# Kernel tuning notes

Measured on AMD Instinct MI355X. Metric: run time of the kernel, lower is better.

The kernel has to match this reference:

```python
import jax, jax.numpy as jnp
import numpy as np

B, N_ATOMS = 64, 127            # graphs, atoms per graph (uniform)
L = N_ATOMS + 1                 # +1 cls token
D_MODEL, NHEAD, NUM_LAYERS, D_FF = 1024, 16, 8, 3072
HEAD_DIM = D_MODEL // NHEAD
MAX_TOKENS = 131                # 121 + 10
NEIGH_VOCAB = 14 + 3            # max_neighbors + 3
DIST_VOCAB = 83 + 3             # max_distance + 3
EPS = 1e-5


def _dist_bins():
    # short_cutoff=0.9, long_cutoff=5.0, precision=0.05; first 3 edges overridden
    b = np.arange(0.9 - 3 * 0.05, 5.0, 0.05)
    b[:3] = [-1.0, 0.0, 0.01]
    return jnp.asarray(b, jnp.float32)  # len 85 -> digitize indices in [0, 85]


def _layer_norm(x, g, b):
    m = jnp.mean(x, -1, keepdims=True)
    v = jnp.var(x, -1, keepdims=True)
    return (x - m) * jax.lax.rsqrt(v + EPS) * g + b


def setup_inputs() -> dict:
    key = jax.random.key(0)
    ks = jax.random.split(key, 16)
    s = 0.02
    z = jax.random.randint(ks[0], (B * N_ATOMS,), 0, 119)
    hgs = jax.random.randint(ks[1], (B * N_ATOMS,), 0, 15)
    pos = jax.random.normal(ks[2], (B * N_ATOMS, 3), jnp.float32) * 3.0
    batch = jnp.repeat(jnp.arange(B, dtype=jnp.int64), N_ATOMS)
    atoms_emb = (jax.random.normal(ks[3], (MAX_TOKENS, D_MODEL), jnp.float32) * s).at[0].set(0.0)  # padding_idx=0
    neigh_emb = (jax.random.normal(ks[4], (NEIGH_VOCAB, D_MODEL), jnp.float32) * s).at[0].set(0.0)
    dist_emb = jax.random.normal(ks[5], (DIST_VOCAB, NHEAD), jnp.float32) * s  # row 0 forced to -inf in reference
    Wqkv = jax.random.normal(ks[6], (D_MODEL, 3 * D_MODEL), jnp.float32) * s
    bqkv = jnp.zeros((3 * D_MODEL,), jnp.float32)
    Wo = jax.random.normal(ks[7], (D_MODEL, D_MODEL), jnp.float32) * s
    bo = jnp.zeros((D_MODEL,), jnp.float32)
    W1 = jax.random.normal(ks[8], (D_MODEL, D_FF), jnp.float32) * s
    b1f = jnp.zeros((D_FF,), jnp.float32)
    W2 = jax.random.normal(ks[9], (D_FF, D_MODEL), jnp.float32) * s
    b2f = jnp.zeros((D_MODEL,), jnp.float32)
    ln1_g = jnp.ones((D_MODEL,), jnp.float32); ln1_b = jnp.zeros((D_MODEL,), jnp.float32)
    ln2_g = jnp.ones((D_MODEL,), jnp.float32); ln2_b = jnp.zeros((D_MODEL,), jnp.float32)
    return dict(z=z, hgs=hgs, pos=pos, batch=batch, atoms_emb=atoms_emb, neigh_emb=neigh_emb,
                dist_emb=dist_emb, Wqkv=Wqkv, bqkv=bqkv, Wo=Wo, bo=bo,
                W1=W1, b1f=b1f, W2=W2, b2f=b2f,
                ln1_g=ln1_g, ln1_b=ln1_b, ln2_g=ln2_g, ln2_b=ln2_b)


def reference(z, hgs, pos, batch, atoms_emb, neigh_emb, dist_emb,
              Wqkv, bqkv, Wo, bo, W1, b1f, W2, b2f, ln1_g, ln1_b, ln2_g, ln2_b):
    # batch is uniform (N_ATOMS per graph, sorted), so per-graph batching == reshape
    zb = z.reshape(B, N_ATOMS).astype(jnp.int32) + 2
    hb = hgs.reshape(B, N_ATOMS).astype(jnp.int32) + 2
    atoms = jnp.concatenate([jnp.ones((B, 1), jnp.int32), zb], axis=1)        # cls token = 1
    neighbors = jnp.concatenate([jnp.zeros((B, 1), jnp.int32), hb], axis=1)   # cls neighbors = 0

    p = pos.reshape(B, N_ATOMS, 3)
    dist = jnp.sqrt(jnp.sum((p[:, None, :, :] - p[:, :, None, :]) ** 2, axis=-1))  # (B,n,n)
    didx = jnp.digitize(dist, _dist_bins()).astype(jnp.int32)                      # self-loop -> 2
    distances = jnp.ones((B, L, L), jnp.int32).at[:, 1:, 1:].set(didx)             # cls row/col = 1

    # neg_inf_idx=0 padding mask row (unused here since no padding -> indices >= 1)
    w_d = dist_emb.at[0].set(-jnp.inf)
    d_mask = w_d[distances].transpose(0, 3, 1, 2)  # (B, H, L, L)

    x = atoms_emb[atoms] + neigh_emb[neighbors]    # (B, L, D)
    scale = 1.0 / jnp.sqrt(jnp.float32(HEAD_DIM))
    for _ in range(NUM_LAYERS):  # shared weights + shared attention bias
        qkv = x @ Wqkv + bqkv
        q, k, v = jnp.split(qkv, 3, axis=-1)
        q = q.reshape(B, L, NHEAD, HEAD_DIM)
        k = k.reshape(B, L, NHEAD, HEAD_DIM)
        v = v.reshape(B, L, NHEAD, HEAD_DIM)
        scores = jnp.einsum('blhd,bmhd->bhlm', q, k) * scale + d_mask
        a = jax.nn.softmax(scores, axis=-1)
        o = jnp.einsum('bhlm,bmhd->blhd', a, v).reshape(B, L, D_MODEL) @ Wo + bo
        x = _layer_norm(x + o, ln1_g, ln1_b)                      # post-norm (norm_first=False)
        h = jax.nn.gelu(x @ W1 + b1f, approximate=False) @ W2 + b2f
        x = _layer_norm(x + h, ln2_g, ln2_b)
    return x[:, 0]  # cls embedding, (B, D_MODEL)
```

## Files before the change

kernel.cpp:

```cpp
#include <hip/hip_runtime.h>
#include <cstdint>
#include <math.h>

typedef unsigned short u16;
typedef __attribute__((ext_vector_type(4))) float f32x4;
typedef __attribute__((ext_vector_type(8))) __bf16 bf16x8;
typedef __attribute__((ext_vector_type(8))) short short8;

typedef __attribute__((address_space(1))) void g_void;
typedef __attribute__((address_space(3))) void l_void;

__device__ __forceinline__ u16 f2bf(float f) {
  uint32_t u = __builtin_bit_cast(uint32_t, f);
  u += 0x7FFFu + ((u >> 16) & 1u);
  return (u16)(u >> 16);
}
__device__ __forceinline__ float bf2f(u16 h) {
  uint32_t u = ((uint32_t)h) << 16;
  return __builtin_bit_cast(float, u);
}

__device__ __forceinline__ void gload16(const void* g, void* l) {
  __builtin_amdgcn_global_load_lds((g_void*)g, (l_void*)l, 16, 0, 0);
}

__device__ __forceinline__ float gelu_exact(float x) {
  float a = x * 0.70710678118654752f;
  float s = fabsf(a);
  float t = __builtin_amdgcn_rcpf(fmaf(0.3275911f, s, 1.0f));
  float p = fmaf(fmaf(fmaf(fmaf(1.061405429f, t, -1.453152027f), t, 1.421413741f), t,
                      -0.284496736f), t, 0.254829592f);
  p *= t;
  float e = __expf(-s * s);
  float er = fmaf(-p, e, 1.0f);
  er = copysignf(er, a);
  return 0.5f * x * (1.0f + er);
}

__global__ void transpose_w(const float* __restrict__ W, u16* __restrict__ Wt, int K, int N) {
  __shared__ float t[32][33];
  const int nb = blockIdx.x * 32, kb = blockIdx.y * 32;
  const int tx = threadIdx.x, ty = threadIdx.y;
#pragma unroll
  for (int i = 0; i < 32; i += 8)
    t[ty + i][tx] = W[(size_t)(kb + ty + i) * N + nb + tx];
  __syncthreads();
#pragma unroll
  for (int i = 0; i < 32; i += 8)
    Wt[(size_t)(nb + ty + i) * K + kb + tx] = f2bf(t[tx][ty + i]);
}

__global__ void embed_k(const int* __restrict__ z, const int* __restrict__ hgs,
                        const float* __restrict__ ae, const float* __restrict__ ne,
                        u16* __restrict__ xb) {
  const int row = blockIdx.x;
  const int b = row >> 7, tl = row & 127;
  int ia = 1, in_ = 0;
  if (tl > 0) { ia = z[b * 127 + tl - 1] + 2; in_ = hgs[b * 127 + tl - 1] + 2; }
  const float* ar = ae + (size_t)ia * 1024;
  const float* nr = ne + (size_t)in_ * 1024;
  for (int c = threadIdx.x; c < 1024; c += 256)
    xb[(size_t)row * 1024 + c] = f2bf(ar[c] + nr[c]);
}

__global__ void mask_k(const float* __restrict__ pos, const float* __restrict__ demb,
                       u16* __restrict__ mask) {
  __shared__ float edges[85];
  __shared__ float dh[86 * 16];
  const int bq = blockIdx.x;
  const int b = bq >> 7, lq = bq & 127;
  const int lk = threadIdx.x;
  if (lk < 85) {
    double e = 0.75 + 0.05 * (double)lk;
    float ef = (float)e;
    if (lk == 0) ef = -1.0f; else if (lk == 1) ef = 0.0f; else if (lk == 2) ef = 0.01f;
    edges[lk] = ef;
  }
  for (int i = lk; i < 86 * 16; i += 128) {
    float v = demb[i];
    if (i < 16) v = -INFINITY;
    dh[i] = v;
  }
  __syncthreads();
  int c;
  if (lq == 0 || lk == 0) {
    c = 1;
  } else {
    const float* pi = pos + ((size_t)b * 127 + lq - 1) * 3;
    const float* pj = pos + ((size_t)b * 127 + lk - 1) * 3;
    const float dx = pi[0] - pj[0], dy = pi[1] - pj[1], dz = pi[2] - pj[2];
    const float d = sqrtf(dx * dx + dy * dy + dz * dz);
    int cnt = 0;
#pragma unroll
    for (int k2 = 0; k2 < 85; ++k2) cnt += (edges[k2] <= d) ? 1 : 0;
    c = cnt;
  }
  const int fr = lk & 15, nn = lk >> 4;
#pragma unroll
  for (int h = 0; h < 16; ++h)
    mask[((((size_t)(b * 16 + h) * 16 + fr) * 128 + lq) << 3) + nn] = f2bf(dh[c * 16 + h]);
}

template <int MODE>
__launch_bounds__(512, 4)
__global__ void gemmS(const u16* __restrict__ A, const u16* __restrict__ Bt,
                      const float* __restrict__ bias,
                      u16* __restrict__ O0, u16* __restrict__ O1, u16* __restrict__ O2,
                      int N, int K) {
  extern __shared__ char lds[];
  constexpr int SLAB = 24576;
  const int tid = threadIdx.x;
  const int w = tid >> 6, l = tid & 63;
  const int wr = w >> 1, wc = w & 1;
  const int nwg = gridDim.x;
  const int wg = (blockIdx.x & 7) * (nwg >> 3) + (blockIdx.x >> 3);
  const int ntn = N >> 7;
  const int bm = wg / ntn, bn = wg - (wg / ntn) * ntn;
  const int NT = K >> 5;

  const int colc = ((((l & 3) << 4) ^ (((l >> 2) & 8) << 2)) >> 1);
  const u16* Ag = A + (size_t)(bm * 256 + w * 16 + (l >> 2)) * K + colc;
  const u16* Bg = Bt + (size_t)(bn * 128 + w * 16 + (l >> 2)) * K + colc;
  const int ldst = w << 10;

  auto stage = [&](int t, char* buf) {
    const int kb = t << 5;
    gload16(Ag + kb, buf + ldst);
    gload16(Ag + (size_t)128 * K + kb, buf + 8192 + ldst);
    gload16(Bg + kb, buf + 16384 + ldst);
  };

  const int lo = ((l & 15) << 6) + (((l >> 4) << 4) ^ ((l & 8) << 2));

  f32x4 acc[4][4];
#pragma unroll
  for (int m = 0; m < 4; ++m)
#pragma unroll
    for (int n = 0; n < 4; ++n) acc[m][n] = f32x4{0.f, 0.f, 0.f, 0.f};

  char* p0 = lds;
  char* p1 = lds + SLAB;
  char* p2 = lds + 2 * SLAB;

  stage(0, p0);
  stage(1, p1);
  asm volatile("s_waitcnt vmcnt(3)" ::: "memory");
  __builtin_amdgcn_s_barrier();

  for (int t = 0; t < NT; ++t) {
    if (t + 2 < NT) stage(t + 2, p2);
    const char* ab = p0 + (wr << 12);
    const char* bb = p0 + 16384 + (wc << 12);
    bf16x8 af[4], bf[4];
#pragma unroll
    for (int m = 0; m < 4; ++m) af[m] = *(const bf16x8*)(ab + (m << 10) + lo);
#pragma unroll
    for (int n = 0; n < 4; ++n) bf[n] = *(const bf16x8*)(bb + (n << 10) + lo);
    __builtin_amdgcn_s_setprio(1);
#pragma unroll
    for (int m = 0; m < 4; ++m)
#pragma unroll
      for (int n = 0; n < 4; ++n)
        acc[m][n] = __builtin_amdgcn_mfma_f32_16x16x32_bf16(af[m], bf[n], acc[m][n], 0, 0, 0);
    __builtin_amdgcn_s_setprio(0);
    if (t + 2 < NT) asm volatile("s_waitcnt vmcnt(3)" ::: "memory");
    else            asm volatile("s_waitcnt vmcnt(0)" ::: "memory");
    __builtin_amdgcn_s_barrier();
    char* tmp = p0; p0 = p1; p1 = p2; p2 = tmp;
  }

  const int fr = l & 15, fq = l >> 4;
  const int colb = bn * 128 + wc * 64;
  const int rowb = bm * 256 + wr * 64;
  float bv[4];
#pragma unroll
  for (int n = 0; n < 4; ++n) bv[n] = bias[colb + n * 16 + fr];
  const int region = colb >> 10;

#pragma unroll
  for (int m = 0; m < 4; ++m) {
#pragma unroll
    for (int n = 0; n < 4; ++n) {
      const int col = colb + n * 16 + fr;
      if (MODE == 0 && region == 2) {
        const int row0_ = rowb + m * 16 + fq * 4;
        const int bI = row0_ >> 7, tl0 = row0_ & 127;
        const int c = col & 1023, h = c >> 6, d = c & 63;
        ushort4 pk;
        pk.x = f2bf(acc[m][n][0] + bv[n]);
        pk.y = f2bf(acc[m][n][1] + bv[n]);
        pk.z = f2bf(acc[m][n][2] + bv[n]);
        pk.w = f2bf(acc[m][n][3] + bv[n]);
        *(ushort4*)&O2[(((size_t)bI * 16 + h) * 64 + d) * 128 + tl0] = pk;
      } else {
#pragma unroll
        for (int j = 0; j < 4; ++j) {
          const int row = rowb + m * 16 + fq * 4 + j;
          float v = acc[m][n][j] + bv[n];
          if (MODE == 2) v = gelu_exact(v);
          if (MODE == 0) {
            const int bI = row >> 7, tl = row & 127;
            const int c = col & 1023, h = c >> 6, d = c & 63;
            if (region == 0) O0[(((size_t)bI * 16 + h) * 128 + tl) * 64 + d] = f2bf(v);
            else             O1[(((size_t)bI * 16 + h) * 128 + tl) * 64 + d] = f2bf(v);
          } else {
            O0[(size_t)row * N + col] = f2bf(v);
          }
        }
      }
    }
  }
}

__launch_bounds__(256, 3)
__global__ void gemm4(const u16* __restrict__ A, const u16* __restrict__ Bt,
                      const float* __restrict__ bias, u16* __restrict__ O,
                      int N, int K) {
  extern __shared__ char lds[];
  constexpr int SLAB = 16384;
  const int tid = threadIdx.x;
  const int w = tid >> 6, l = tid & 63;
  const int wr = w >> 1, wc = w & 1;
  const int nwg = gridDim.x;
  const int wg = (blockIdx.x & 7) * (nwg >> 3) + (blockIdx.x >> 3);
  const int ntn = N >> 7;
  const int bm = wg / ntn, bn = wg - (wg / ntn) * ntn;
  const int NT = K >> 5;

  const int colc = ((((l & 3) << 4) ^ (((l >> 2) & 8) << 2)) >> 1);
  const u16* Ag = A + (size_t)(bm * 128 + w * 16 + (l >> 2)) * K + colc;
  const u16* Bg = Bt + (size_t)(bn * 128 + w * 16 + (l >> 2)) * K + colc;
  const int ldst = w << 10;

  auto stage = [&](int t, char* buf) {
    const int kb = t << 5;
    gload16(Ag + kb, buf + ldst);
    gload16(Ag + (size_t)64 * K + kb, buf + 4096 + ldst);
    gload16(Bg + kb, buf + 8192 + ldst);
    gload16(Bg + (size_t)64 * K + kb, buf + 12288 + ldst);
  };

  const int lo = ((l & 15) << 6) + (((l >> 4) << 4) ^ ((l & 8) << 2));

  f32x4 acc[4][4];
#pragma unroll
  for (int m = 0; m < 4; ++m)
#pragma unroll
    for (int n = 0; n < 4; ++n) acc[m][n] = f32x4{0.f, 0.f, 0.f, 0.f};

  char* p0 = lds;
  char* p1 = lds + SLAB;
  char* p2 = lds + 2 * SLAB;

  stage(0, p0);
  stage(1, p1);
  asm volatile("s_waitcnt vmcnt(4)" ::: "memory");
  __builtin_amdgcn_s_barrier();

  for (int t = 0; t < NT; ++t) {
    if (t + 2 < NT) stage(t + 2, p2);
    const char* ab = p0 + (wr << 12);
    const char* bb = p0 + 8192 + (wc << 12);
    bf16x8 af[4], bf[4];
#pragma unroll
    for (int m = 0; m < 4; ++m) af[m] = *(const bf16x8*)(ab + (m << 10) + lo);
#pragma unroll
    for (int n = 0; n < 4; ++n) bf[n] = *(const bf16x8*)(bb + (n << 10) + lo);
    __builtin_amdgcn_s_setprio(1);
#pragma unroll
    for (int m = 0; m < 4; ++m)
#pragma unroll
      for (int n = 0; n < 4; ++n)
        acc[m][n] = __builtin_amdgcn_mfma_f32_16x16x32_bf16(af[m], bf[n], acc[m][n], 0, 0, 0);
    __builtin_amdgcn_s_setprio(0);
    if (t + 2 < NT) asm volatile("s_waitcnt vmcnt(4)" ::: "memory");
    else            asm volatile("s_waitcnt vmcnt(0)" ::: "memory");
    __builtin_amdgcn_s_barrier();
    char* tmp = p0; p0 = p1; p1 = p2; p2 = tmp;
  }

  const int fr = l & 15, fq = l >> 4;
  const int colb = bn * 128 + wc * 64;
  const int rowb = bm * 128 + wr * 64;
  float bv[4];
#pragma unroll
  for (int n = 0; n < 4; ++n) bv[n] = bias[colb + n * 16 + fr];
#pragma unroll
  for (int m = 0; m < 4; ++m)
#pragma unroll
    for (int n = 0; n < 4; ++n) {
      const int col = colb + n * 16 + fr;
#pragma unroll
      for (int j = 0; j < 4; ++j) {
        const int row = rowb + m * 16 + fq * 4 + j;
        O[(size_t)row * N + col] = f2bf(acc[m][n][j] + bv[n]);
      }
    }
}

__launch_bounds__(256)
__global__ void attn_kernel(const u16* __restrict__ Qg, const u16* __restrict__ Kg,
                            const u16* __restrict__ Vg,
                            const u16* __restrict__ mask,
                            u16* __restrict__ Og) {
  __shared__ u16 QK[2 * 128 * 64];
  __shared__ u16 Vt[64 * 128];
  const int tid = threadIdx.x;
  const int wv = tid >> 6;
  const int l = tid & 63;
  const int bh = blockIdx.x;
  const int b = bh >> 4;

  const char* Qs = (const char*)(Qg + (size_t)bh * 8192);
  const char* Ks = (const char*)(Kg + (size_t)bh * 8192);
  const char* Vs = (const char*)(Vg + (size_t)bh * 8192);
  char* QKb = (char*)QK;
  char* Vtb = (char*)Vt;
#pragma unroll
  for (int it = 0; it < 4; ++it) {
    const int r = it * 32 + (tid >> 3);
    const int cb = (tid & 7) * 16;
    const int sw = cb ^ ((r & 7) << 4);
    *(uint4*)(QKb + r * 128 + sw) = *(const uint4*)(Qs + r * 128 + cb);
    *(uint4*)(QKb + 16384 + r * 128 + sw) = *(const uint4*)(Ks + r * 128 + cb);
  }
#pragma unroll
  for (int it = 0; it < 4; ++it) {
    const int r = it * 16 + (tid >> 4);
    const int cb = (tid & 15) * 16;
    const int sw = cb ^ ((r & 7) << 4);
    *(uint4*)(Vtb + r * 256 + sw) = *(const uint4*)(Vs + r * 256 + cb);
  }
  __syncthreads();

  f32x4 s[2][8];
#pragma unroll
  for (int m = 0; m < 2; ++m)
#pragma unroll
    for (int n = 0; n < 8; ++n) s[m][n] = f32x4{0.f, 0.f, 0.f, 0.f};
#pragma unroll
  for (int kk = 0; kk < 2; ++kk) {
    bf16x8 qa[2], kb[8];
#pragma unroll
    for (int m = 0; m < 2; ++m) {
      const int qr = wv * 32 + m * 16 + (l & 15);
      qa[m] = *(const bf16x8*)(QKb + qr * 128 + ((kk * 64 + (l >> 4) * 16) ^ ((qr & 7) << 4)));
    }
#pragma unroll
    for (int n = 0; n < 8; ++n) {
      const int kr = n * 16 + (l & 15);
      kb[n] = *(const bf16x8*)(QKb + 16384 + kr * 128 + ((kk * 64 + (l >> 4) * 16) ^ ((kr & 7) << 4)));
    }
#pragma unroll
    for (int m = 0; m < 2; ++m)
#pragma unroll
      for (int n = 0; n < 8; ++n)
        s[m][n] = __builtin_amdgcn_mfma_f32_16x16x32_bf16(qa[m], kb[n], s[m][n], 0, 0, 0);
  }

  const u16* mb2 = mask + (((size_t)bh * 16 + (l & 15)) << 10);
  float rinv[2][4];
#pragma unroll
  for (int m = 0; m < 2; ++m) {
#pragma unroll
    for (int j = 0; j < 4; ++j) {
      const int lq = wv * 32 + m * 16 + (l >> 4) * 4 + j;
      const short8 mv = *(const short8*)(mb2 + lq * 8);
      float vals[8];
#pragma unroll
      for (int n = 0; n < 8; ++n)
        vals[n] = fmaf(s[m][n][j], 0.125f, bf2f((u16)mv[n]));
      float mx = vals[0];
#pragma unroll
      for (int n = 1; n < 8; ++n) mx = fmaxf(mx, vals[n]);
#pragma unroll
      for (int o = 1; o < 16; o <<= 1) mx = fmaxf(mx, __shfl_xor(mx, o, 64));
      float sum = 0.f;
#pragma unroll
      for (int n = 0; n < 8; ++n) { vals[n] = expf(vals[n] - mx); sum += vals[n]; }
#pragma unroll
      for (int o = 1; o < 16; o <<= 1) sum += __shfl_xor(sum, o, 64);
      rinv[m][j] = 1.f / sum;
#pragma unroll
      for (int n = 0; n < 8; ++n) s[m][n][j] = vals[n];
    }
  }
  __syncthreads();
  char* Pb = QKb + wv * 8192;
#pragma unroll
  for (int m = 0; m < 2; ++m)
#pragma unroll
    for (int n = 0; n < 8; ++n)
#pragma unroll
      for (int j = 0; j < 4; ++j) {
        const int pr = m * 16 + (l >> 4) * 4 + j;
        const int pc = (n * 16 + (l & 15)) * 2;
        *(u16*)(Pb + pr * 256 + (pc ^ ((pr & 7) << 4))) = f2bf(s[m][n][j]);
      }
  __syncthreads();

  f32x4 o_[2][4];
#pragma unroll
  for (int m = 0; m < 2; ++m)
#pragma unroll
    for (int n = 0; n < 4; ++n) o_[m][n] = f32x4{0.f, 0.f, 0.f, 0.f};
#pragma unroll
  for (int ks = 0; ks < 4; ++ks) {
    bf16x8 pa[2], vb[4];
#pragma unroll
    for (int m = 0; m < 2; ++m) {
      const int pr = m * 16 + (l & 15);
      pa[m] = *(const bf16x8*)(Pb + pr * 256 + ((ks * 64 + (l >> 4) * 16) ^ ((pr & 7) << 4)));
    }
#pragma unroll
    for (int n = 0; n < 4; ++n) {
      const int vr = n * 16 + (l & 15);
      vb[n] = *(const bf16x8*)(Vtb + vr * 256 + ((ks * 64 + (l >> 4) * 16) ^ ((vr & 7) << 4)));
    }
#pragma unroll
    for (int m = 0; m < 2; ++m)
#pragma unroll
      for (int n = 0; n < 4; ++n)
        o_[m][n] = __builtin_amdgcn_mfma_f32_16x16x32_bf16(pa[m], vb[n], o_[m][n], 0, 0, 0);
  }
  const int h = bh & 15;
#pragma unroll
  for (int m = 0; m < 2; ++m)
#pragma unroll
    for (int n = 0; n < 4; ++n)
#pragma unroll
      for (int j = 0; j < 4; ++j) {
        const int lo2 = wv * 32 + m * 16 + (l >> 4) * 4 + j;
        const int d = n * 16 + (l & 15);
        Og[((size_t)b * 128 + lo2) * 1024 + h * 64 + d] = f2bf(o_[m][n][j] * rinv[m][j]);
      }
}

__launch_bounds__(256)
__global__ void ln_res(u16* __restrict__ xb, const u16* __restrict__ o,
                       const float* __restrict__ gam, const float* __restrict__ bet,
                       float* __restrict__ cls_out) {
  const int row = blockIdx.x * 4 + (threadIdx.x >> 6);
  const int l = threadIdx.x & 63;
  const size_t base = (size_t)row * 1024 + l * 16;
  const int c0 = l * 16;
  float v[16], gv[16], bb[16];
  const short8 xa = *(const short8*)(xb + base);
  const short8 xc = *(const short8*)(xb + base + 8);
  const short8 oa = *(const short8*)(o + base);
  const short8 oc = *(const short8*)(o + base + 8);
#pragma unroll
  for (int i = 0; i < 4; ++i) {
    *(float4*)&gv[i * 4] = *(const float4*)(gam + c0 + i * 4);
    *(float4*)&bb[i * 4] = *(const float4*)(bet + c0 + i * 4);
  }
  float s = 0.f, sq = 0.f;
#pragma unroll
  for (int i = 0; i < 8; ++i) {
    v[i] = bf2f((u16)xa[i]) + bf2f((u16)oa[i]);
    v[i + 8] = bf2f((u16)xc[i]) + bf2f((u16)oc[i]);
  }
#pragma unroll
  for (int i = 0; i < 16; ++i) { s += v[i]; sq += v[i] * v[i]; }
#pragma unroll
  for (int off = 1; off < 64; off <<= 1) {
    s += __shfl_xor(s, off, 64);
    sq += __shfl_xor(sq, off, 64);
  }
  const float mean = s * (1.f / 1024.f);
  const float var = sq * (1.f / 1024.f) - mean * mean;
  const float rstd = rsqrtf(var + 1e-5f);
  short8 ra, rc;
#pragma unroll
  for (int i = 0; i < 8; ++i) {
    const float ya = (v[i] - mean) * rstd * gv[i] + bb[i];
    const float yc = (v[i + 8] - mean) * rstd * gv[i + 8] + bb[i + 8];
    ra[i] = (short)f2bf(ya);
    rc[i] = (short)f2bf(yc);
    if ((row & 127) == 0) {
      cls_out[(size_t)(row >> 7) * 1024 + c0 + i] = ya;
      cls_out[(size_t)(row >> 7) * 1024 + c0 + 8 + i] = yc;
    }
  }
  *(short8*)(xb + base) = ra;
  *(short8*)(xb + base + 8) = rc;
}

extern "C" void kernel_launch(void* const* d_in, const int* in_sizes, int n_in,
                              void* d_out, int out_size, void* d_ws, size_t ws_size,
                              hipStream_t stream) {
  const int* z = (const int*)d_in[0];
  const int* hgs = (const int*)d_in[1];
  const float* pos = (const float*)d_in[2];
  const float* atoms_emb = (const float*)d_in[4];
  const float* neigh_emb = (const float*)d_in[5];
  const float* dist_emb = (const float*)d_in[6];
  const float* Wqkv = (const float*)d_in[7];
  const float* bqkv = (const float*)d_in[8];
  const float* Wo = (const float*)d_in[9];
  const float* bo = (const float*)d_in[10];
  const float* W1 = (const float*)d_in[11];
  const float* b1f = (const float*)d_in[12];
  const float* W2 = (const float*)d_in[13];
  const float* b2f = (const float*)d_in[14];
  const float* ln1g = (const float*)d_in[15];
  const float* ln1b = (const float*)d_in[16];
  const float* ln2g = (const float*)d_in[17];
  const float* ln2b = (const float*)d_in[18];

  size_t off = 0;
  char* wsb = (char*)d_ws;
  auto alc = [&](size_t bytes) { void* p = wsb + off; off += (bytes + 255) & ~(size_t)255; return p; };
  u16* xb = (u16*)alc(8192ull * 1024 * 2);
  u16* q = (u16*)alc(8192ull * 1024 * 2);
  u16* k = (u16*)alc(8192ull * 1024 * 2);
  u16* v = (u16*)alc(8192ull * 1024 * 2);
  u16* proj = (u16*)alc(8192ull * 1024 * 2);
  u16* big = (u16*)alc(8192ull * 3072 * 2);
  u16* wqkvt = (u16*)alc(3072ull * 1024 * 2);
  u16* wot = (u16*)alc(1024ull * 1024 * 2);
  u16* w1t = (u16*)alc(3072ull * 1024 * 2);
  u16* w2t = (u16*)alc(1024ull * 3072 * 2);
  u16* mask = (u16*)alc(64ull * 16 * 16 * 128 * 8 * 2);

  hipFuncSetAttribute((const void*)gemmS<0>, hipFuncAttributeMaxDynamicSharedMemorySize, 73728);
  hipFuncSetAttribute((const void*)gemmS<2>, hipFuncAttributeMaxDynamicSharedMemorySize, 73728);
  hipFuncSetAttribute((const void*)gemm4, hipFuncAttributeMaxDynamicSharedMemorySize, 49152);

  transpose_w<<<dim3(96, 32), dim3(32, 8), 0, stream>>>(Wqkv, wqkvt, 1024, 3072);
  transpose_w<<<dim3(32, 32), dim3(32, 8), 0, stream>>>(Wo, wot, 1024, 1024);
  transpose_w<<<dim3(96, 32), dim3(32, 8), 0, stream>>>(W1, w1t, 1024, 3072);
  transpose_w<<<dim3(32, 96), dim3(32, 8), 0, stream>>>(W2, w2t, 3072, 1024);
  embed_k<<<8192, 256, 0, stream>>>(z, hgs, atoms_emb, neigh_emb, xb);
  mask_k<<<8192, 128, 0, stream>>>(pos, dist_emb, mask);

  float* cls = (float*)d_out;
  for (int layer = 0; layer < 8; ++layer) {
    gemmS<0><<<768, 512, 73728, stream>>>(xb, wqkvt, bqkv, q, k, v, 3072, 1024);
    attn_kernel<<<1024, 256, 0, stream>>>(q, k, v, mask, big);
    gemm4<<<512, 256, 49152, stream>>>(big, wot, bo, proj, 1024, 1024);
    ln_res<<<2048, 256, 0, stream>>>(xb, proj, ln1g, ln1b, cls);
    gemmS<2><<<768, 512, 73728, stream>>>(xb, w1t, b1f, big, nullptr, nullptr, 3072, 1024);
    gemm4<<<512, 256, 49152, stream>>>(big, w2t, b2f, proj, 1024, 3072);
    ln_res<<<2048, 256, 0, stream>>>(xb, proj, ln2g, ln2b, cls);
  }
}
```

Measured before the change: 2.211 ms.

## Deepen gemm4 pipeline to four stages and preload attention mask into accumulators

The N=1024 GEMM grows from a 3-buffer to a 4-buffer LDS ring with three tiles in flight and a 4x-unrolled loop. Occupancy drops from 3 to 2 blocks per CU to make room for the extra LDS. The attention bias is now stored pre-scaled by 8 in a transposed layout and loaded straight into the QK^T accumulators, so the MFMA adds it and the separate mask load after softmax scaling goes away. One __syncthreads between the P write and the PV read is dropped; this relies on each wave reading only its own P rows, which is a correctness risk if any other data dependence was covered by that barrier.

```diff
diff --git a/kernel.cpp b/kernel.cpp
--- a/kernel.cpp
+++ b/kernel.cpp
@@ -95,10 +95,9 @@
     for (int k2 = 0; k2 < 85; ++k2) cnt += (edges[k2] <= d) ? 1 : 0;
     c = cnt;
   }
-  const int fr = lk & 15, nn = lk >> 4;
 #pragma unroll
   for (int h = 0; h < 16; ++h)
-    mask[((((size_t)(b * 16 + h) * 16 + fr) * 128 + lq) << 3) + nn] = f2bf(dh[c * 16 + h]);
+    mask[((size_t)(b * 16 + h) << 14) + lk * 128 + lq] = f2bf(dh[c * 16 + h] * 8.0f);
 }
 
 template <int MODE>
@@ -212,12 +211,11 @@
   }
 }
 
-__launch_bounds__(256, 3)
-__global__ void gemm4(const u16* __restrict__ A, const u16* __restrict__ Bt,
-                      const float* __restrict__ bias, u16* __restrict__ O,
-                      int N, int K) {
+__launch_bounds__(256, 2)
+__global__ void gemm4r(const u16* __restrict__ A, const u16* __restrict__ Bt,
+                       const float* __restrict__ bias, u16* __restrict__ O,
+                       int N, int K) {
   extern __shared__ char lds[];
-  constexpr int SLAB = 16384;
   const int tid = threadIdx.x;
   const int w = tid >> 6, l = tid & 63;
   const int wr = w >> 1, wc = w & 1;
@@ -232,7 +230,8 @@
   const u16* Bg = Bt + (size_t)(bn * 128 + w * 16 + (l >> 2)) * K + colc;
   const int ldst = w << 10;
 
-  auto stage = [&](int t, char* buf) {
+  auto stage = [&](int t) {
+    char* buf = lds + ((t & 3) << 14);
     const int kb = t << 5;
     gload16(Ag + kb, buf + ldst);
     gload16(Ag + (size_t)64 * K + kb, buf + 4096 + ldst);
@@ -248,19 +247,9 @@
 #pragma unroll
     for (int n = 0; n < 4; ++n) acc[m][n] = f32x4{0.f, 0.f, 0.f, 0.f};
 
-  char* p0 = lds;
-  char* p1 = lds + SLAB;
-  char* p2 = lds + 2 * SLAB;
-
-  stage(0, p0);
-  stage(1, p1);
-  asm volatile("s_waitcnt vmcnt(4)" ::: "memory");
-  __builtin_amdgcn_s_barrier();
-
-  for (int t = 0; t < NT; ++t) {
-    if (t + 2 < NT) stage(t + 2, p2);
-    const char* ab = p0 + (wr << 12);
-    const char* bb = p0 + 8192 + (wc << 12);
+  auto compute = [&](int bi) {
+    const char* ab = lds + (bi << 14) + (wr << 12);
+    const char* bb = lds + (bi << 14) + 8192 + (wc << 12);
     bf16x8 af[4], bf[4];
 #pragma unroll
     for (int m = 0; m < 4; ++m) af[m] = *(const bf16x8*)(ab + (m << 10) + lo);
@@ -273,11 +262,32 @@
       for (int n = 0; n < 4; ++n)
         acc[m][n] = __builtin_amdgcn_mfma_f32_16x16x32_bf16(af[m], bf[n], acc[m][n], 0, 0, 0);
     __builtin_amdgcn_s_setprio(0);
-    if (t + 2 < NT) asm volatile("s_waitcnt vmcnt(4)" ::: "memory");
-    else            asm volatile("s_waitcnt vmcnt(0)" ::: "memory");
-    __builtin_amdgcn_s_barrier();
-    char* tmp = p0; p0 = p1; p1 = p2; p2 = tmp;
-  }
+  };
+
+  stage(0); stage(1); stage(2);
+  asm volatile("s_waitcnt vmcnt(8)" ::: "memory");
+  __builtin_amdgcn_s_barrier();
+
+  for (int t4 = 0; t4 + 4 < NT; t4 += 4) {
+#pragma unroll
+    for (int u = 0; u < 4; ++u) {
+      stage(t4 + u + 3);
+      compute(u);
+      asm volatile("s_waitcnt vmcnt(8)" ::: "memory");
+      __builtin_amdgcn_s_barrier();
+    }
+  }
+  stage(NT - 1);
+  compute(0);
+  asm volatile("s_waitcnt vmcnt(8)" ::: "memory");
+  __builtin_amdgcn_s_barrier();
+  compute(1);
+  asm volatile("s_waitcnt vmcnt(4)" ::: "memory");
+  __builtin_amdgcn_s_barrier();
+  compute(2);
+  asm volatile("s_waitcnt vmcnt(0)" ::: "memory");
+  __builtin_amdgcn_s_barrier();
+  compute(3);
 
   const int fr = l & 15, fq = l >> 4;
   const int colb = bn * 128 + wc * 64;
@@ -331,13 +341,21 @@
     const int sw = cb ^ ((r & 7) << 4);
     *(uint4*)(Vtb + r * 256 + sw) = *(const uint4*)(Vs + r * 256 + cb);
   }
+
+  const u16* m8 = mask + ((size_t)bh << 14);
+  f32x4 s[2][8];
+#pragma unroll
+  for (int m = 0; m < 2; ++m) {
+    const int r0 = wv * 32 + m * 16 + (l >> 4) * 4;
+#pragma unroll
+    for (int n = 0; n < 8; ++n) {
+      const int col = n * 16 + (l & 15);
+      const ushort4 mv = *(const ushort4*)(m8 + col * 128 + r0);
+      s[m][n] = f32x4{bf2f(mv.x), bf2f(mv.y), bf2f(mv.z), bf2f(mv.w)};
+    }
+  }
   __syncthreads();
 
-  f32x4 s[2][8];
-#pragma unroll
-  for (int m = 0; m < 2; ++m)
-#pragma unroll
-    for (int n = 0; n < 8; ++n) s[m][n] = f32x4{0.f, 0.f, 0.f, 0.f};
 #pragma unroll
   for (int kk = 0; kk < 2; ++kk) {
     bf16x8 qa[2], kb[8];
@@ -358,18 +376,15 @@
         s[m][n] = __builtin_amdgcn_mfma_f32_16x16x32_bf16(qa[m], kb[n], s[m][n], 0, 0, 0);
   }
 
-  const u16* mb2 = mask + (((size_t)bh * 16 + (l & 15)) << 10);
   float rinv[2][4];
 #pragma unroll
   for (int m = 0; m < 2; ++m) {
 #pragma unroll
     for (int j = 0; j < 4; ++j) {
-      const int lq = wv * 32 + m * 16 + (l >> 4) * 4 + j;
-      const short8 mv = *(const short8*)(mb2 + lq * 8);
       float vals[8];
 #pragma unroll
       for (int n = 0; n < 8; ++n)
-        vals[n] = fmaf(s[m][n][j], 0.125f, bf2f((u16)mv[n]));
+        vals[n] = s[m][n][j] * 0.125f;
       float mx = vals[0];
 #pragma unroll
       for (int n = 1; n < 8; ++n) mx = fmaxf(mx, vals[n]);
@@ -397,7 +412,6 @@
         const int pc = (n * 16 + (l & 15)) * 2;
         *(u16*)(Pb + pr * 256 + (pc ^ ((pr & 7) << 4))) = f2bf(s[m][n][j]);
       }
-  __syncthreads();
 
   f32x4 o_[2][4];
 #pragma unroll
@@ -521,11 +535,11 @@
   u16* wot = (u16*)alc(1024ull * 1024 * 2);
   u16* w1t = (u16*)alc(3072ull * 1024 * 2);
   u16* w2t = (u16*)alc(1024ull * 3072 * 2);
-  u16* mask = (u16*)alc(64ull * 16 * 16 * 128 * 8 * 2);
+  u16* mask = (u16*)alc(64ull * 16 * 128 * 128 * 2);
 
   hipFuncSetAttribute((const void*)gemmS<0>, hipFuncAttributeMaxDynamicSharedMemorySize, 73728);
   hipFuncSetAttribute((const void*)gemmS<2>, hipFuncAttributeMaxDynamicSharedMemorySize, 73728);
-  hipFuncSetAttribute((const void*)gemm4, hipFuncAttributeMaxDynamicSharedMemorySize, 49152);
+  hipFuncSetAttribute((const void*)gemm4r, hipFuncAttributeMaxDynamicSharedMemorySize, 65536);
 
   transpose_w<<<dim3(96, 32), dim3(32, 8), 0, stream>>>(Wqkv, wqkvt, 1024, 3072);
   transpose_w<<<dim3(32, 32), dim3(32, 8), 0, stream>>>(Wo, wot, 1024, 1024);
@@ -538,10 +552,10 @@
   for (int layer = 0; layer < 8; ++layer) {
     gemmS<0><<<768, 512, 73728, stream>>>(xb, wqkvt, bqkv, q, k, v, 3072, 1024);
     attn_kernel<<<1024, 256, 0, stream>>>(q, k, v, mask, big);
-    gemm4<<<512, 256, 49152, stream>>>(big, wot, bo, proj, 1024, 1024);
+    gemm4r<<<512, 256, 65536, stream>>>(big, wot, bo, proj, 1024, 1024);
     ln_res<<<2048, 256, 0, stream>>>(xb, proj, ln1g, ln1b, cls);
     gemmS<2><<<768, 512, 73728, stream>>>(xb, w1t, b1f, big, nullptr, nullptr, 3072, 1024);
-    gemm4<<<512, 256, 49152, stream>>>(big, w2t, b2f, proj, 1024, 3072);
+    gemm4r<<<512, 256, 65536, stream>>>(big, w2t, b2f, proj, 1024, 3072);
     ln_res<<<2048, 256, 0, stream>>>(xb, proj, ln2g, ln2b, cls);
   }
 }
```

After: 2.295 ms. 3.8% more time.
